# Performance work log

Hardware: AMD Instinct MI355X
Metric: run time of the kernel (lower is better)

The kernel has to match this reference:

```python
import jax, jax.numpy as jnp
import numpy as np

NUM_HEADS = 16
HEAD_DIM = 128  # embed_dim 2048 / 16 heads
ROPE_BASE = 10000.0


def rope_sincos(seq_len, dim, dtype=jnp.float32):
    # sin/cos tables of shape [seq_len, dim//2]
    inv_freq = 1.0 / (ROPE_BASE ** (jnp.arange(0, dim, 2, dtype=dtype) / dim))
    t = jnp.arange(seq_len, dtype=dtype)
    freqs = jnp.einsum('s,f->sf', t, inv_freq)
    return jnp.sin(freqs), jnp.cos(freqs)


def apply_rotary_pos_emb(x, sin, cos):
    # x: [b, s, h, d]; sin/cos: [s, d//2] -> rotate-half RoPE
    x1, x2 = jnp.split(x, 2, axis=-1)
    sin = sin[None, :, None, :]
    cos = cos[None, :, None, :]
    return jnp.concatenate([x1 * cos - x2 * sin, x2 * cos + x1 * sin], axis=-1)


def setup_inputs() -> dict:
    key = jax.random.key(0)
    k1, k2 = jax.random.split(key)
    B, S, E = 4, 2048, 2048
    x = jax.random.normal(k1, (B, S, E), dtype=jnp.float32)
    Wqkv = jax.random.normal(k2, (E, 3 * E), dtype=jnp.float32) * (E ** -0.5)
    mask = jnp.ones((B, S), dtype=bool)
    return {"x": x, "mask": mask, "Wqkv": Wqkv}


def reference(x, mask, Wqkv):
    B, S, E = x.shape
    H, D = NUM_HEADS, HEAD_DIM
    qkv = x @ Wqkv                                  # [B, S, 3*E]
    q, k, v = jnp.split(qkv, 3, axis=-1)
    q = q.reshape(B, S, H, D)
    k = k.reshape(B, S, H, D)
    v = v.reshape(B, S, H, D)
    sin, cos = rope_sincos(S, D, dtype=x.dtype)
    q = apply_rotary_pos_emb(q, sin, cos)
    k = apply_rotary_pos_emb(k, sin, cos)
    attn = jnp.einsum('bqhd,bkhd->bhqk', q, k) / jnp.sqrt(jnp.asarray(D, x.dtype))
    m = jnp.broadcast_to(mask[:, None, None, :], (B, H, S, S))
    attn = jnp.where(m, attn, jnp.asarray(-jnp.inf, attn.dtype))
    attn = jax.nn.softmax(attn, axis=-1)
    out = jnp.einsum('bhqk,bkhd->bqhd', attn, v)
    return out.reshape(B, S, H * D)
```

## Files before the change

### kernel.cpp

```cpp
#include <hip/hip_runtime.h>

typedef unsigned short u16;
typedef _Float16 f16x8 __attribute__((ext_vector_type(8)));
typedef float f32x4 __attribute__((ext_vector_type(4)));

__device__ __forceinline__ float h2f(u16 u) {
  _Float16 h;
  __builtin_memcpy(&h, &u, 2);
  return (float)h;
}
__device__ __forceinline__ u16 f2h(float f) {
  _Float16 h = (_Float16)f;
  u16 u;
  __builtin_memcpy(&u, &h, 2);
  return u;
}

__device__ __forceinline__ void async_copy16(const u16* g, u16* l) {
  __builtin_amdgcn_global_load_lds((__attribute__((address_space(1))) void*)g,
                                   (__attribute__((address_space(3))) void*)l,
                                   16, 0, 0);
}

__global__ __launch_bounds__(256) void convert_f32_f16(const float* __restrict__ in,
                                                       u16* __restrict__ out) {
  unsigned int i = (blockIdx.x * 256u + threadIdx.x) * 4u;
  float4 v = *(const float4*)&in[i];
  ushort4 o;
  o.x = f2h(v.x); o.y = f2h(v.y); o.z = f2h(v.z); o.w = f2h(v.w);
  *(ushort4*)&out[i] = o;
}

__global__ __launch_bounds__(256) void transpose_f32_f16(const float* __restrict__ in,
                                                         u16* __restrict__ out,
                                                         int rows, int cols, int tiles_c) {
  __shared__ u16 tile[64][65];
  int tr = blockIdx.x / tiles_c, tc = blockIdx.x % tiles_c;
  int r0 = tr * 64, c0 = tc * 64;
  int lr = threadIdx.x >> 4;
  int lc = (threadIdx.x & 15) * 4;
#pragma unroll
  for (int i = 0; i < 4; ++i) {
    int r = lr + i * 16;
    float4 v = *(const float4*)&in[(size_t)(r0 + r) * cols + c0 + lc];
    tile[r][lc] = f2h(v.x); tile[r][lc + 1] = f2h(v.y);
    tile[r][lc + 2] = f2h(v.z); tile[r][lc + 3] = f2h(v.w);
  }
  __syncthreads();
#pragma unroll
  for (int i = 0; i < 4; ++i) {
    int r = lr + i * 16;
    ushort4 v;
    v.x = tile[lc + 0][r]; v.y = tile[lc + 1][r]; v.z = tile[lc + 2][r]; v.w = tile[lc + 3][r];
    *(ushort4*)&out[(size_t)(c0 + r) * rows + r0 + lc] = v;
  }
}

__global__ __launch_bounds__(256) void transpose_u16(const u16* __restrict__ in,
                                                     u16* __restrict__ out,
                                                     int rows, int cols, int tiles_c) {
  __shared__ u16 tile[64][65];
  size_t base = (size_t)blockIdx.y * (size_t)rows * (size_t)cols;
  int tr = blockIdx.x / tiles_c, tc = blockIdx.x % tiles_c;
  int r0 = tr * 64, c0 = tc * 64;
  int lr = threadIdx.x >> 4;
  int lc = (threadIdx.x & 15) * 4;
#pragma unroll
  for (int i = 0; i < 4; ++i) {
    int r = lr + i * 16;
    ushort4 v = *(const ushort4*)&in[base + (size_t)(r0 + r) * cols + c0 + lc];
    tile[r][lc] = v.x; tile[r][lc + 1] = v.y; tile[r][lc + 2] = v.z; tile[r][lc + 3] = v.w;
  }
  __syncthreads();
#pragma unroll
  for (int i = 0; i < 4; ++i) {
    int r = lr + i * 16;
    ushort4 v;
    v.x = tile[lc + 0][r]; v.y = tile[lc + 1][r]; v.z = tile[lc + 2][r]; v.w = tile[lc + 3][r];
    *(ushort4*)&out[base + (size_t)(c0 + r) * rows + r0 + lc] = v;
  }
}

__global__ __launch_bounds__(512, 2) void qkv_gemm(const u16* __restrict__ x, const u16* __restrict__ Wt,
                                                   u16* __restrict__ Qb, u16* __restrict__ Kb,
                                                   u16* __restrict__ Vn) {
  __shared__ __align__(16) u16 lds[65536];

  int tid = threadIdx.x, lane = tid & 63, w = tid >> 6;
  int quad = lane >> 4, l15 = lane & 15;
  int wm = w >> 2, wn = w & 3;
  int bid = blockIdx.x;
  int swz = (bid & 7) * 96 + (bid >> 3);
  int nb = swz % 24, mb = swz / 24;
  int m0 = mb * 256, n0 = nb * 256;

  int xo = 8 * ((lane & 7) ^ (lane >> 3));
  int stg0 = (w * 16 + (lane >> 3)) * 2048 + xo;
  int stg1 = (w * 16 + 8 + (lane >> 3)) * 2048 + xo;
  int wst0 = w * 1024;
  int wst1 = w * 1024 + 512;
  const u16* pA0 = x  + (size_t)m0 * 2048;
  const u16* pA1 = x  + (size_t)(m0 + 128) * 2048;
  const u16* pB0 = Wt + (size_t)n0 * 2048;
  const u16* pB1 = Wt + (size_t)(n0 + 128) * 2048;

  int fA = (l15 & 7) << 3;
  int aoff[8], boff[8];
#pragma unroll
  for (int mt = 0; mt < 4; ++mt)
#pragma unroll
    for (int ks = 0; ks < 2; ++ks)
      aoff[mt * 2 + ks] = wm * 8192 + (mt * 16 + l15) * 64 + ((ks * 32 + quad * 8) ^ fA);
#pragma unroll
  for (int nt4 = 0; nt4 < 4; ++nt4)
#pragma unroll
    for (int ks = 0; ks < 2; ++ks)
      boff[nt4 * 2 + ks] = (2 + (wn >> 1)) * 8192 + ((wn & 1) * 64 + nt4 * 16 + l15) * 64 +
                           ((ks * 32 + quad * 8) ^ fA);

  f16x8 a[8], b[8];
  f32x4 acc[8][4];
#pragma unroll
  for (int i = 0; i < 8; ++i)
#pragma unroll
    for (int j = 0; j < 4; ++j) acc[i][j] = (f32x4){0.f, 0.f, 0.f, 0.f};

#define STAGE_A(BUF, HALF, T) do {                                                   \
    const u16* g_ = (HALF) ? pA1 : pA0;                                              \
    async_copy16(g_ + stg0 + (T) * 64, &lds[(BUF) * 32768 + (HALF) * 8192 + wst0]);  \
    async_copy16(g_ + stg1 + (T) * 64, &lds[(BUF) * 32768 + (HALF) * 8192 + wst1]);  \
  } while (0)
#define STAGE_B(BUF, HALF, T) do {                                                        \
    const u16* g_ = (HALF) ? pB1 : pB0;                                                   \
    async_copy16(g_ + stg0 + (T) * 64, &lds[(BUF) * 32768 + (2 + (HALF)) * 8192 + wst0]); \
    async_copy16(g_ + stg1 + (T) * 64, &lds[(BUF) * 32768 + (2 + (HALF)) * 8192 + wst1]); \
  } while (0)
#define LDA(BUF, QROW) do {                                                  \
    _Pragma("unroll") for (int q_ = 0; q_ < 8; ++q_)                         \
      a[q_] = *(const f16x8*)&lds[(BUF) * 32768 + (QROW) * 4096 + aoff[q_]]; \
  } while (0)
#define LDB(BUF, QCOL) do {                                                          \
    _Pragma("unroll") for (int q_ = 0; q_ < 4; ++q_)                                 \
      b[(QCOL) * 4 + q_] = *(const f16x8*)&lds[(BUF) * 32768 + boff[(QCOL) * 4 + q_]]; \
  } while (0)
#define MM(QROW, QCOL) do {                                                           \
    __builtin_amdgcn_s_setprio(1);                                                    \
    _Pragma("unroll") for (int ks_ = 0; ks_ < 2; ++ks_)                               \
    _Pragma("unroll") for (int mt_ = 0; mt_ < 4; ++mt_)                               \
    _Pragma("unroll") for (int nt_ = 0; nt_ < 2; ++nt_)                               \
      acc[(QROW) * 4 + mt_][(QCOL) * 2 + nt_] =                                       \
          __builtin_amdgcn_mfma_f32_16x16x32_f16(a[mt_ * 2 + ks_],                    \
                                                 b[(QCOL) * 4 + nt_ * 2 + ks_],       \
                                                 acc[(QROW) * 4 + mt_][(QCOL) * 2 + nt_], 0, 0, 0); \
    __builtin_amdgcn_s_setprio(0);                                                    \
  } while (0)
#define BAR __builtin_amdgcn_s_barrier()

#define DO_TILE(BUF, T) do {                                                 \
             \
    LDA(BUF, 0);                                                             \
    LDB(BUF, 0);                                                             \
    if ((T) + 1 < 32) STAGE_A((BUF) ^ 1, 0, (T) + 1);                        \
    BAR;                                                                     \
    MM(0, 0);                                                                \
    BAR;                                                                     \
                        \
    LDB(BUF, 1);                                                             \
    if ((T) + 1 < 32) STAGE_A((BUF) ^ 1, 1, (T) + 1);                        \
    BAR;                                                                     \
    MM(0, 1);                                                                \
    BAR;                                                                     \
                       \
    LDA(BUF, 1);                                                             \
    if ((T) + 2 < 32) STAGE_B(BUF, 0, (T) + 2);                              \
    BAR;                                                                     \
    MM(1, 1);                                                                \
    BAR;                                                                     \
                \
    if ((T) + 2 < 32) STAGE_B(BUF, 1, (T) + 2);                              \
    BAR;                                                                     \
    MM(1, 0);                                                                \
    if ((T) < 30) { asm volatile("s_waitcnt vmcnt(4)" ::: "memory"); }       \
    else          { asm volatile("s_waitcnt vmcnt(0)" ::: "memory"); }       \
    BAR;                                                                     \
  } while (0)

  STAGE_A(0, 0, 0);
  STAGE_A(0, 1, 0);
  STAGE_B(0, 0, 0);
  STAGE_B(0, 1, 0);
  STAGE_B(1, 0, 1);
  STAGE_B(1, 1, 1);
  asm volatile("s_waitcnt vmcnt(4)" ::: "memory");
  BAR;

  for (int t = 0; t < 32; t += 2) {
    DO_TILE(0, t);
    DO_TILE(1, t + 1);
  }

  int tnum = n0 >> 11;
  u16* dst = (tnum == 0) ? Qb : ((tnum == 1) ? Kb : Vn);
#pragma unroll
  for (int i = 0; i < 8; ++i) {
#pragma unroll
    for (int j = 0; j < 4; ++j) {
      int col = n0 + wn * 64 + (j >> 1) * 32 + (j & 1) * 16 + l15;
      int h = (col >> 7) & 15, d = col & 127;
#pragma unroll
      for (int r = 0; r < 4; ++r) {
        int row = m0 + wm * 128 + (i >> 2) * 64 + (i & 3) * 16 + quad * 4 + r;
        int bb = row >> 11, s = row & 2047;
        dst[((size_t)(bb * 16 + h) * 2048 + s) * 128 + d] = f2h(acc[i][j][r]);
      }
    }
  }
#undef STAGE_A
#undef STAGE_B
#undef LDA
#undef LDB
#undef MM
#undef BAR
#undef DO_TILE
}

__global__ __launch_bounds__(256) void rope_k_kernel(u16* __restrict__ Kb) {
  unsigned int idx = blockIdx.x * 256u + threadIdx.x;
  int j = idx & 63;
  int s = (idx >> 6) & 2047;
  int bh = (idx >> 17) & 63;
  size_t off = ((size_t)bh * 2048 + s) * 128;
  float x1 = h2f(Kb[off + j]);
  float x2 = h2f(Kb[off + j + 64]);
  float inv_freq = powf(10000.0f, -(float)j * (1.0f / 64.0f));
  float ang = (float)s * inv_freq;
  float sn, cs;
  __sincosf(ang, &sn, &cs);
  Kb[off + j]      = f2h(x1 * cs - x2 * sn);
  Kb[off + j + 64] = f2h(x2 * cs + x1 * sn);
}

#define ATTN_SCALE 0.08838834764831845f
#define PK_OFF 4608
#define PV_OFF 12800

__global__ __launch_bounds__(256, 3) void attn_kernel(const u16* __restrict__ Qb,
                                                      const u16* __restrict__ Kb,
                                                      const u16* __restrict__ Vt,
                                                      float* __restrict__ out) {
  __shared__ __align__(16) u16 smem[20992];

  int tid = threadIdx.x, lane = tid & 63, w = tid >> 6;
  int quad = lane >> 4, l15 = lane & 15;
  int qt = blockIdx.x & 15, bh = blockIdx.x >> 4;
  int q0 = qt * 128;
  const u16* Qg = Qb + ((size_t)bh * 2048 + q0) * 128;
  const u16* Kg = Kb + (size_t)bh * 2048 * 128;
  const u16* Vg = Vt + (size_t)bh * 128 * 2048;

  int kSrc[2], vSrc[2], kDst[2], vDst[2];
#pragma unroll
  for (int c = 0; c < 2; ++c) {
    int krow = w * 8 + c * 4 + quad;
    kSrc[c] = krow * 128 + ((l15 ^ (krow & 15)) * 8);
    kDst[c] = (w * 8 + c * 4) * 128 + lane * 8;
    int vrow = w * 32 + c * 16 + (lane >> 2);
    vSrc[c] = vrow * 2048 + (((lane & 3) ^ ((vrow >> 1) & 3)) * 8);
    vDst[c] = (w * 32 + c * 16) * 32 + lane * 8;
  }

#pragma unroll
  for (int c = 0; c < 8; ++c) {
    int chunk = w * 8 + c;
    async_copy16(Qg + chunk * 512 + lane * 8, &smem[chunk * 512]);
  }
  __syncthreads();

  f16x8 qf[2][4];
#pragma unroll
  for (int mt = 0; mt < 2; ++mt)
#pragma unroll
    for (int ks = 0; ks < 4; ++ks)
      qf[mt][ks] = *(const f16x8*)&smem[(w * 32 + mt * 16 + l15) * 128 + ks * 32 + quad * 8];
#pragma unroll
  for (int mt = 0; mt < 2; ++mt) {
    float srow = (float)(q0 + w * 32 + mt * 16 + l15);
#pragma unroll
    for (int ks = 0; ks < 2; ++ks)
#pragma unroll
      for (int e = 0; e < 8; ++e) {
        int j = ks * 32 + quad * 8 + e;
        float inv_freq = powf(10000.0f, -(float)j * (1.0f / 64.0f));
        float ang = srow * inv_freq;
        float sn, cs;
        __sincosf(ang, &sn, &cs);
        float x1 = (float)qf[mt][ks][e];
        float x2 = (float)qf[mt][ks + 2][e];
        qf[mt][ks][e]     = (_Float16)(x1 * cs - x2 * sn);
        qf[mt][ks + 2][e] = (_Float16)(x2 * cs + x1 * sn);
      }
  }
  __syncthreads();

#pragma unroll
  for (int c = 0; c < 2; ++c) {
    async_copy16(Kg + kSrc[c], &smem[PK_OFF + kDst[c]]);
    async_copy16(Vg + vSrc[c], &smem[PV_OFF + vDst[c]]);
  }

  f32x4 o[2][8];
#pragma unroll
  for (int mt = 0; mt < 2; ++mt)
#pragma unroll
    for (int nto = 0; nto < 8; ++nto) o[mt][nto] = (f32x4){0.f, 0.f, 0.f, 0.f};
  float lrun[2][4];
#pragma unroll
  for (int mt = 0; mt < 2; ++mt)
#pragma unroll
    for (int r = 0; r < 4; ++r) lrun[mt][r] = 0.f;

  for (int kb = 0; kb < 64; ++kb) {
    __syncthreads();
    int cur = kb & 1, nxt = cur ^ 1;

    if (kb + 1 < 64) {
      const u16* Kt = Kg + (size_t)(kb + 1) * 4096;
      const u16* Vk = Vg + (size_t)(kb + 1) * 32;
#pragma unroll
      for (int c = 0; c < 2; ++c) {
        async_copy16(Kt + kSrc[c], &smem[PK_OFF + nxt * 4096 + kDst[c]]);
        async_copy16(Vk + vSrc[c], &smem[PV_OFF + nxt * 4096 + vDst[c]]);
      }
    }

    const u16* Kl = &smem[PK_OFF + cur * 4096];
    const u16* Vl = &smem[PV_OFF + cur * 4096];

    f32x4 sa[2][2];
#pragma unroll
    for (int mt = 0; mt < 2; ++mt)
#pragma unroll
      for (int nt = 0; nt < 2; ++nt) sa[mt][nt] = (f32x4){0.f, 0.f, 0.f, 0.f};
#pragma unroll
    for (int ks = 0; ks < 4; ++ks) {
      f16x8 kf[2];
#pragma unroll
      for (int nt = 0; nt < 2; ++nt)
        kf[nt] = *(const f16x8*)&Kl[(nt * 16 + l15) * 128 + (((ks * 4 + quad) ^ l15) * 8)];
#pragma unroll
      for (int mt = 0; mt < 2; ++mt)
#pragma unroll
        for (int nt = 0; nt < 2; ++nt)
          sa[mt][nt] = __builtin_amdgcn_mfma_f32_16x16x32_f16(qf[mt][ks], kf[nt], sa[mt][nt], 0, 0, 0);
    }

#pragma unroll
    for (int mt = 0; mt < 2; ++mt)
#pragma unroll
      for (int r = 0; r < 4; ++r) {
        float p0 = __expf(sa[mt][0][r] * ATTN_SCALE);
        float p1 = __expf(sa[mt][1][r] * ATTN_SCALE);
        lrun[mt][r] += p0 + p1;
        u16* prow = &smem[(w * 32 + mt * 16 + quad * 4 + r) * 36];
        prow[l15]      = f2h(p0);
        prow[16 + l15] = f2h(p1);
      }

    f16x8 pf[2];
#pragma unroll
    for (int mt = 0; mt < 2; ++mt)
      pf[mt] = *(const f16x8*)&smem[(w * 32 + mt * 16 + l15) * 36 + quad * 8];
#pragma unroll
    for (int nto = 0; nto < 8; ++nto) {
      f16x8 vf = *(const f16x8*)&Vl[(nto * 16 + l15) * 32 + ((quad ^ ((l15 >> 1) & 3)) * 8)];
#pragma unroll
      for (int mt = 0; mt < 2; ++mt)
        o[mt][nto] = __builtin_amdgcn_mfma_f32_16x16x32_f16(pf[mt], vf, o[mt][nto], 0, 0, 0);
    }
  }

  int b = bh >> 4, h = bh & 15;
#pragma unroll
  for (int mt = 0; mt < 2; ++mt)
#pragma unroll
    for (int r = 0; r < 4; ++r) {
      float s = lrun[mt][r];
      s += __shfl_xor(s, 1); s += __shfl_xor(s, 2);
      s += __shfl_xor(s, 4); s += __shfl_xor(s, 8);
      float inv = 1.0f / s;
      int sq = q0 + w * 32 + mt * 16 + quad * 4 + r;
      size_t rowaddr = ((size_t)b * 2048 + sq) * 2048 + (size_t)h * 128;
#pragma unroll
      for (int nto = 0; nto < 8; ++nto)
        out[rowaddr + nto * 16 + l15] = o[mt][nto][r] * inv;
    }
}

extern "C" void kernel_launch(void* const* d_in, const int* in_sizes, int n_in,
                              void* d_out, int out_size, void* d_ws, size_t ws_size,
                              hipStream_t stream) {
  const float* x    = (const float*)d_in[0];
  const float* Wqkv = (const float*)d_in[2];
  float* out = (float*)d_out;

  u16* ws = (u16*)d_ws;
  u16* Xh = ws;
  u16* Wt = Xh + 16777216;
  u16* Qb = Wt + 12582912;
  u16* Kb = Qb + 16777216;
  u16* Vn = Kb + 16777216;
  u16* Vt = Xh;
  (void)in_sizes; (void)n_in; (void)out_size; (void)ws_size;

  convert_f32_f16<<<dim3(16384), 256, 0, stream>>>(x, Xh);
  transpose_f32_f16<<<dim3(32 * 96), 256, 0, stream>>>(Wqkv, Wt, 2048, 6144, 96);
  qkv_gemm<<<dim3(32 * 24), dim3(512), 0, stream>>>(Xh, Wt, Qb, Kb, Vn);
  rope_k_kernel<<<dim3(32768), 256, 0, stream>>>(Kb);
  transpose_u16<<<dim3(64, 64), 256, 0, stream>>>(Vn, Vt, 2048, 128, 2);
  attn_kernel<<<dim3(1024), 256, 0, stream>>>(Qb, Kb, Vt, out);
}
```

Measured before the change: 567.8 us.

## Fuse K RoPE and V transpose into QKV GEMM epilogue

The QKV GEMM epilogue now applies RoPE to K by staging the tile in LDS and writing vectorized rotated rows, and writes V directly in transposed layout. This removes the separate rope_k_kernel and transpose_u16 launches and their extra global round trips. The block swizzle for L2 locality is dropped, and powf is replaced by exp2f for the inverse frequencies. The V epilogue writes strided 8-byte chunks, which may be less coalesced, and the dropped swizzle may hurt GEMM cache reuse.

Measured after the change: 537.3 us. 1.06x faster.

```diff
diff --git a/kernel.cpp b/kernel.cpp
--- a/kernel.cpp
+++ b/kernel.cpp
@@ -3,6 +3,8 @@
 typedef unsigned short u16;
 typedef _Float16 f16x8 __attribute__((ext_vector_type(8)));
 typedef float f32x4 __attribute__((ext_vector_type(4)));
+
+#define LOG2_10000 13.287712379549449f
 
 __device__ __forceinline__ float h2f(u16 u) {
   _Float16 h;
@@ -56,42 +58,15 @@
   }
 }
 
-__global__ __launch_bounds__(256) void transpose_u16(const u16* __restrict__ in,
-                                                     u16* __restrict__ out,
-                                                     int rows, int cols, int tiles_c) {
-  __shared__ u16 tile[64][65];
-  size_t base = (size_t)blockIdx.y * (size_t)rows * (size_t)cols;
-  int tr = blockIdx.x / tiles_c, tc = blockIdx.x % tiles_c;
-  int r0 = tr * 64, c0 = tc * 64;
-  int lr = threadIdx.x >> 4;
-  int lc = (threadIdx.x & 15) * 4;
-#pragma unroll
-  for (int i = 0; i < 4; ++i) {
-    int r = lr + i * 16;
-    ushort4 v = *(const ushort4*)&in[base + (size_t)(r0 + r) * cols + c0 + lc];
-    tile[r][lc] = v.x; tile[r][lc + 1] = v.y; tile[r][lc + 2] = v.z; tile[r][lc + 3] = v.w;
-  }
-  __syncthreads();
-#pragma unroll
-  for (int i = 0; i < 4; ++i) {
-    int r = lr + i * 16;
-    ushort4 v;
-    v.x = tile[lc + 0][r]; v.y = tile[lc + 1][r]; v.z = tile[lc + 2][r]; v.w = tile[lc + 3][r];
-    *(ushort4*)&out[base + (size_t)(c0 + r) * rows + r0 + lc] = v;
-  }
-}
-
 __global__ __launch_bounds__(512, 2) void qkv_gemm(const u16* __restrict__ x, const u16* __restrict__ Wt,
                                                    u16* __restrict__ Qb, u16* __restrict__ Kb,
-                                                   u16* __restrict__ Vn) {
+                                                   u16* __restrict__ Vt) {
   __shared__ __align__(16) u16 lds[65536];
 
   int tid = threadIdx.x, lane = tid & 63, w = tid >> 6;
   int quad = lane >> 4, l15 = lane & 15;
   int wm = w >> 2, wn = w & 3;
-  int bid = blockIdx.x;
-  int swz = (bid & 7) * 96 + (bid >> 3);
-  int nb = swz % 24, mb = swz / 24;
+  int nb = blockIdx.x % 24, mb = blockIdx.x / 24;
   int m0 = mb * 256, n0 = nb * 256;
 
   int xo = 8 * ((lane & 7) ^ (lane >> 3));
@@ -200,19 +175,72 @@
   }
 
   int tnum = n0 >> 11;
-  u16* dst = (tnum == 0) ? Qb : ((tnum == 1) ? Kb : Vn);
-#pragma unroll
-  for (int i = 0; i < 8; ++i) {
-#pragma unroll
-    for (int j = 0; j < 4; ++j) {
-      int col = n0 + wn * 64 + (j >> 1) * 32 + (j & 1) * 16 + l15;
-      int h = (col >> 7) & 15, d = col & 127;
-#pragma unroll
-      for (int r = 0; r < 4; ++r) {
-        int row = m0 + wm * 128 + (i >> 2) * 64 + (i & 3) * 16 + quad * 4 + r;
-        int bb = row >> 11, s = row & 2047;
-        dst[((size_t)(bb * 16 + h) * 2048 + s) * 128 + d] = f2h(acc[i][j][r]);
-      }
+  if (tnum == 2) {
+#pragma unroll
+    for (int i = 0; i < 8; ++i)
+#pragma unroll
+      for (int j = 0; j < 4; ++j) {
+        int col = n0 + wn * 64 + (j >> 1) * 32 + (j & 1) * 16 + l15;
+        int h = (col >> 7) & 15, d = col & 127;
+        int row0 = m0 + wm * 128 + (i >> 2) * 64 + (i & 3) * 16 + quad * 4;
+        int bb = row0 >> 11, s0 = row0 & 2047;
+        ushort4 v;
+        v.x = f2h(acc[i][j][0]); v.y = f2h(acc[i][j][1]);
+        v.z = f2h(acc[i][j][2]); v.w = f2h(acc[i][j][3]);
+        *(ushort4*)&Vt[((size_t)(bb * 16 + h) * 128 + d) * 2048 + s0] = v;
+      }
+  } else if (tnum == 0) {
+#pragma unroll
+    for (int i = 0; i < 8; ++i)
+#pragma unroll
+      for (int j = 0; j < 4; ++j) {
+        int col = n0 + wn * 64 + (j >> 1) * 32 + (j & 1) * 16 + l15;
+        int h = (col >> 7) & 15, d = col & 127;
+#pragma unroll
+        for (int r = 0; r < 4; ++r) {
+          int row = m0 + wm * 128 + (i >> 2) * 64 + (i & 3) * 16 + quad * 4 + r;
+          int bb = row >> 11, s = row & 2047;
+          Qb[((size_t)(bb * 16 + h) * 2048 + s) * 128 + d] = f2h(acc[i][j][r]);
+        }
+      }
+  } else {
+#pragma unroll
+    for (int i = 0; i < 8; ++i)
+#pragma unroll
+      for (int j = 0; j < 4; ++j) {
+        int lcol = wn * 64 + (j >> 1) * 32 + (j & 1) * 16 + l15;
+        int lrow0 = wm * 128 + (i >> 2) * 64 + (i & 3) * 16 + quad * 4;
+#pragma unroll
+        for (int r = 0; r < 4; ++r)
+          lds[(lrow0 + r) * 256 + lcol] = f2h(acc[i][j][r]);
+      }
+    __syncthreads();
+    int bb = m0 >> 11, sbase = m0 & 2047;
+    int h0 = (n0 & 2047) >> 7;
+    int jbase = (l15 & 7) * 8;
+    bool hiHalf = l15 >= 8;
+    float invf[8];
+#pragma unroll
+    for (int e = 0; e < 8; ++e)
+      invf[e] = exp2f((float)(jbase + e) * (-LOG2_10000 / 64.0f));
+#pragma unroll
+    for (int it = 0; it < 16; ++it) {
+      int combo = it * 32 + w * 4 + quad;
+      int lrow = combo & 255, hh = combo >> 8;
+      int s = sbase + lrow;
+      const u16* base = &lds[lrow * 256 + hh * 128 + jbase];
+      f16x8 xlo = *(const f16x8*)(base);
+      f16x8 xhi = *(const f16x8*)(base + 64);
+      f16x8 ov;
+#pragma unroll
+      for (int e = 0; e < 8; ++e) {
+        float sn, cs;
+        __sincosf((float)s * invf[e], &sn, &cs);
+        float x1 = (float)xlo[e], x2 = (float)xhi[e];
+        float o = hiHalf ? (x2 * cs + x1 * sn) : (x1 * cs - x2 * sn);
+        ov[e] = (_Float16)o;
+      }
+      *(f16x8*)&Kb[((size_t)(bb * 16 + h0 + hh) * 2048 + s) * 128 + l15 * 8] = ov;
     }
   }
 #undef STAGE_A
@@ -224,22 +252,6 @@
 #undef DO_TILE
 }
 
-__global__ __launch_bounds__(256) void rope_k_kernel(u16* __restrict__ Kb) {
-  unsigned int idx = blockIdx.x * 256u + threadIdx.x;
-  int j = idx & 63;
-  int s = (idx >> 6) & 2047;
-  int bh = (idx >> 17) & 63;
-  size_t off = ((size_t)bh * 2048 + s) * 128;
-  float x1 = h2f(Kb[off + j]);
-  float x2 = h2f(Kb[off + j + 64]);
-  float inv_freq = powf(10000.0f, -(float)j * (1.0f / 64.0f));
-  float ang = (float)s * inv_freq;
-  float sn, cs;
-  __sincosf(ang, &sn, &cs);
-  Kb[off + j]      = f2h(x1 * cs - x2 * sn);
-  Kb[off + j + 64] = f2h(x2 * cs + x1 * sn);
-}
-
 #define ATTN_SCALE 0.08838834764831845f
 #define PK_OFF 4608
 #define PV_OFF 12800
@@ -290,7 +302,7 @@
 #pragma unroll
       for (int e = 0; e < 8; ++e) {
         int j = ks * 32 + quad * 8 + e;
-        float inv_freq = powf(10000.0f, -(float)j * (1.0f / 64.0f));
+        float inv_freq = exp2f((float)j * (-LOG2_10000 / 64.0f));
         float ang = srow * inv_freq;
         float sn, cs;
         __sincosf(ang, &sn, &cs);
@@ -408,14 +420,11 @@
   u16* Wt = Xh + 16777216;
   u16* Qb = Wt + 12582912;
   u16* Kb = Qb + 16777216;
-  u16* Vn = Kb + 16777216;
-  u16* Vt = Xh;
+  u16* Vt = Kb + 16777216;
   (void)in_sizes; (void)n_in; (void)out_size; (void)ws_size;
 
   convert_f32_f16<<<dim3(16384), 256, 0, stream>>>(x, Xh);
   transpose_f32_f16<<<dim3(32 * 96), 256, 0, stream>>>(Wqkv, Wt, 2048, 6144, 96);
-  qkv_gemm<<<dim3(32 * 24), dim3(512), 0, stream>>>(Xh, Wt, Qb, Kb, Vn);
-  rope_k_kernel<<<dim3(32768), 256, 0, stream>>>(Kb);
-  transpose_u16<<<dim3(64, 64), 256, 0, stream>>>(Vn, Vt, 2048, 128, 2);
+  qkv_gemm<<<dim3(32 * 24), dim3(512), 0, stream>>>(Xh, Wt, Qb, Kb, Vt);
   attn_kernel<<<dim3(1024), 256, 0, stream>>>(Qb, Kb, Vt, out);
 }
```
